# Performance work log

Measured on AMD Instinct MI355X. Metric: run time of the kernel, lower is better.

## Reference

```python
import jax, jax.numpy as jnp
import numpy as np

D_MODEL, D_STATE, D_CONV, EXPAND, DT_RANK = 2048, 16, 4, 2, 128
D_INNER = EXPAND * D_MODEL
BATCH, SEQLEN = 4, 2048


def setup_inputs() -> dict:
    key = jax.random.key(0)
    ks = jax.random.split(key, 10)
    s = lambda fan_in: 1.0 / np.sqrt(fan_in)
    hidden_states = jax.random.normal(ks[0], (BATCH, SEQLEN, D_MODEL), jnp.float32)
    W_in = jax.random.normal(ks[1], (2 * D_INNER, D_MODEL), jnp.float32) * s(D_MODEL)
    conv_w = jax.random.normal(ks[2], (D_INNER, D_CONV), jnp.float32) * s(D_CONV)
    conv_b = jax.random.normal(ks[3], (D_INNER,), jnp.float32) * 0.02
    W_x = jax.random.normal(ks[4], (DT_RANK + 2 * D_STATE, D_INNER), jnp.float32) * s(D_INNER)
    W_dt = jax.random.normal(ks[5], (D_INNER, DT_RANK), jnp.float32) * s(DT_RANK)
    # dt bias init so softplus(dt+bias) lands in a realistic small-dt range
    dt = jnp.exp(jax.random.uniform(ks[6], (D_INNER,)) * (np.log(0.1) - np.log(1e-3)) + np.log(1e-3))
    dt_bias = dt + jnp.log(-jnp.expm1(-dt))  # inverse softplus
    # A = -[1..d_state] per channel (standard S4D-real init)
    A_log = jnp.log(jnp.tile(jnp.arange(1, D_STATE + 1, dtype=jnp.float32), (D_INNER, 1)))
    D = jnp.ones((D_INNER,), jnp.float32)
    W_out = jax.random.normal(ks[7], (D_MODEL, D_INNER), jnp.float32) * s(D_INNER)
    return dict(hidden_states=hidden_states, W_in=W_in, conv_w=conv_w, conv_b=conv_b,
                W_x=W_x, W_dt=W_dt, dt_bias=dt_bias, A_log=A_log, D=D, W_out=W_out)


def _mamba_forward(hidden_states, W_in, conv_w, conv_b, W_x, W_dt, dt_bias, A_log, D, W_out):
    B_, L, _ = hidden_states.shape
    d_inner, d_state = A_log.shape
    dt_rank = W_dt.shape[1]

    # in_proj: (B,L,2*d_inner)
    xz = jnp.einsum('bld,ed->ble', hidden_states, W_in)
    x, z = jnp.split(xz, 2, axis=-1)              # each (B,L,d_inner)

    # depthwise causal conv1d over time
    x_bdl = jnp.transpose(x, (0, 2, 1))           # (B,d_inner,L)
    x_conv = jax.lax.conv_general_dilated(
        x_bdl, conv_w[:, None, :], window_strides=(1,),
        padding=[(conv_w.shape[-1] - 1, 0)],
        feature_group_count=d_inner,
        dimension_numbers=('NCH', 'OIH', 'NCH'))
    x_conv = x_conv + conv_b[None, :, None]
    xact = jax.nn.silu(jnp.transpose(x_conv, (0, 2, 1)))   # (B,L,d_inner)

    # x_proj -> dt, B, C
    x_dbl = jnp.einsum('bld,ed->ble', xact, W_x)
    dt_lr, Bm, Cm = jnp.split(x_dbl, [dt_rank, dt_rank + d_state], axis=-1)
    dt = jnp.einsum('blr,dr->bld', dt_lr, W_dt)            # (B,L,d_inner)
    delta = jax.nn.softplus(dt + dt_bias)                   # (B,L,d_inner)

    A = -jnp.exp(A_log)                                     # (d_inner,d_state)

    # selective scan over time (time-major xs)
    def step(h, inp):
        u_t, dlt_t, b_t, c_t = inp                          # (B,d),(B,d),(B,n),(B,n)
        dA = jnp.exp(dlt_t[..., None] * A)                  # (B,d,n)
        h = h * dA + (dlt_t * u_t)[..., None] * b_t[:, None, :]
        y_t = jnp.einsum('bdn,bn->bd', h, c_t)
        return h, y_t

    xs = (jnp.transpose(xact, (1, 0, 2)),
          jnp.transpose(delta, (1, 0, 2)),
          jnp.transpose(Bm, (1, 0, 2)),
          jnp.transpose(Cm, (1, 0, 2)))
    h0 = jnp.zeros((B_, d_inner, d_state), xact.dtype)
    _, ys = jax.lax.scan(step, h0, xs)                      # ys: (L,B,d_inner)
    y = jnp.transpose(ys, (1, 0, 2)) + D * xact             # skip via D
    y = y * jax.nn.silu(z)                                  # gating

    return jnp.einsum('bld,od->blo', y, W_out)              # out_proj


def reference(hidden_states, W_in, conv_w, conv_b, W_x, W_dt, dt_bias, A_log, D, W_out):
    return _mamba_forward(hidden_states, W_in, conv_w, conv_b, W_x, W_dt,
                          dt_bias, A_log, D, W_out)
```

## Files before the change

### kernel.cpp

```cpp
#include <hip/hip_runtime.h>
#include <hip/hip_bf16.h>
#include <math.h>

#define D_MODEL 2048
#define D_STATE 16
#define D_CONV  4
#define DT_RANK 128
#define D_INNER 4096
#define BATCH   4
#define SEQLEN  2048
#define BL      (BATCH * SEQLEN)

#define NCHUNK 8
#define CHUNK  (SEQLEN / NCHUNK)
#define SCH    32
#define NTILE  (CHUNK / SCH)

typedef __hip_bfloat16 bf16;
typedef __attribute__((ext_vector_type(8))) short  short8;
typedef __attribute__((ext_vector_type(4))) float  f32x4;

__device__ __forceinline__ float bf2f(bf16 v) { return __bfloat162float(v); }
__device__ __forceinline__ bf16  f2bf(float v) { return __float2bfloat16(v); }
__device__ __forceinline__ float us2f(unsigned short v) {
    return __uint_as_float((unsigned)v << 16);
}
__device__ __forceinline__ void st1(float* p, float v) { *p = v; }
__device__ __forceinline__ void st1(bf16* p, float v)  { *p = f2bf(v); }
__device__ __forceinline__ float fast_rcp(float x) { return __builtin_amdgcn_rcpf(x); }

__device__ __forceinline__ void async_cp16(const void* g, void* l) {
    __builtin_amdgcn_global_load_lds(
        (const __attribute__((address_space(1))) void*)g,
        (__attribute__((address_space(3))) void*)l, 16, 0, 0);
}

__device__ __forceinline__ float quad_sum(float p) {
    int q;
    q = __builtin_amdgcn_update_dpp(0, __float_as_int(p), 0xB1, 0xF, 0xF, false);
    p += __int_as_float(q);
    q = __builtin_amdgcn_update_dpp(0, __float_as_int(p), 0x4E, 0xF, 0xF, false);
    p += __int_as_float(q);
    return p;
}

template <int EPI, typename TC>
__global__ __launch_bounds__(256) void gemm_mfma_nt(
    const bf16* __restrict__ A, const bf16* __restrict__ B,
    TC* __restrict__ C, int M, int N, int K, int lda, int ldb, int ldc,
    const float* __restrict__ bias, bf16* __restrict__ aux,
    float* __restrict__ aux2)
{
    __shared__ bf16 As[128][64];
    __shared__ bf16 Bs[128][64];

    const int tid  = threadIdx.x;
    const int lane = tid & 63;
    const int wave = tid >> 6;
    const int wm   = (wave >> 1) * 64;
    const int wn   = (wave & 1) * 64;

    const int m0 = blockIdx.x * 128;
    const int n0 = blockIdx.y * 128;

    f32x4 acc[4][4] = {};

    const int srow = lane >> 3;
    const int scol = (lane & 7) * 8;

    for (int k0 = 0; k0 < K; k0 += 64) {
        __syncthreads();
#pragma unroll
        for (int i = 0; i < 4; ++i) {
            int seg = wave * 4 + i;
            int row = seg * 8 + srow;
            async_cp16(A + (size_t)(m0 + row) * lda + k0 + scol, &As[seg * 8][0]);
            async_cp16(B + (size_t)(n0 + row) * ldb + k0 + scol, &Bs[seg * 8][0]);
        }
        __syncthreads();

#pragma unroll
        for (int kk = 0; kk < 64; kk += 32) {
            short8 a[4], b[4];
            const int fr = lane & 15;
            const int fk = kk + (lane >> 4) * 8;
#pragma unroll
            for (int i = 0; i < 4; ++i) {
                a[i] = *(const short8*)&As[wm + i * 16 + fr][fk];
                b[i] = *(const short8*)&Bs[wn + i * 16 + fr][fk];
            }
#pragma unroll
            for (int i = 0; i < 4; ++i)
#pragma unroll
                for (int j = 0; j < 4; ++j)
                    acc[i][j] = __builtin_amdgcn_mfma_f32_16x16x32_bf16(
                        a[i], b[j], acc[i][j], 0, 0, 0);
        }
    }

#pragma unroll
    for (int i = 0; i < 4; ++i) {
        int row = m0 + wm + i * 16 + (lane >> 4) * 4;
#pragma unroll
        for (int j = 0; j < 4; ++j) {
            int col = n0 + wn + j * 16 + (lane & 15);
#pragma unroll
            for (int r = 0; r < 4; ++r) {
                float v = acc[i][j][r];
                if (EPI == 0) {
                    st1(C + (size_t)(row + r) * ldc + col, v);
                } else if (EPI == 1) {
                    if (col < DT_RANK)
                        aux[(size_t)(row + r) * DT_RANK + col] = f2bf(v);
                    else if (col < DT_RANK + 2 * D_STATE)
                        aux2[(size_t)(row + r) * (2 * D_STATE) + (col - DT_RANK)] = v;
                } else {
                    float x  = v + bias[col];
                    float sp = fmaxf(x, 0.f) + __logf(1.f + __expf(-fabsf(x)));
                    ((bf16*)C)[(size_t)(row + r) * ldc + col] = f2bf(sp);
                }
            }
        }
    }
}

__global__ void cvt_f32_bf16(const float* __restrict__ src,
                             bf16* __restrict__ dst, int n)
{
    int i = (blockIdx.x * blockDim.x + threadIdx.x) * 4;
    if (i >= n) return;
    float4 v = *(const float4*)(src + i);
    bf16 o[4] = { f2bf(v.x), f2bf(v.y), f2bf(v.z), f2bf(v.w) };
    *(ushort4*)(dst + i) = *(ushort4*)o;
}

__global__ void cvt_pad_wx(const float* __restrict__ src, bf16* __restrict__ dst)
{
    int i = (blockIdx.x * blockDim.x + threadIdx.x) * 4;
    if (i >= 256 * D_INNER) return;
    int row = i / D_INNER;
    bf16 o[4] = {};
    if (row < DT_RANK + 2 * D_STATE) {
        float4 v = *(const float4*)(src + i);
        o[0] = f2bf(v.x); o[1] = f2bf(v.y); o[2] = f2bf(v.z); o[3] = f2bf(v.w);
    }
    *(ushort4*)(dst + i) = *(ushort4*)o;
}

__global__ void conv_silu(const bf16* __restrict__ X,
                          const float* __restrict__ conv_w,
                          const float* __restrict__ conv_b,
                          bf16* __restrict__ xact)
{
    unsigned idx = blockIdx.x * blockDim.x + threadIdx.x;
    if (idx >= (unsigned)BL * (D_INNER / 8)) return;
    int c8 = (idx & (D_INNER / 8 - 1)) * 8;
    unsigned bl = idx >> 9;
    int l = bl & (SEQLEN - 1);
    int b = bl >> 11;

    float acc[8];
    float4 wv[8];
#pragma unroll
    for (int j = 0; j < 8; ++j) {
        acc[j] = conv_b[c8 + j];
        wv[j]  = *(const float4*)(conv_w + (c8 + j) * 4);
    }
#pragma unroll
    for (int t = 0; t < D_CONV; ++t) {
        int ll = l - (D_CONV - 1) + t;
        if (ll >= 0) {
            short8 xv = *(const short8*)(X + ((size_t)b * SEQLEN + ll) * D_INNER + c8);
#pragma unroll
            for (int j = 0; j < 8; ++j)
                acc[j] = fmaf(us2f((unsigned short)xv[j]), (&wv[j].x)[t], acc[j]);
        }
    }
    bf16 o[8];
#pragma unroll
    for (int j = 0; j < 8; ++j)
        o[j] = f2bf(acc[j] * fast_rcp(1.f + __expf(-acc[j])));
    *(short8*)(xact + (size_t)bl * D_INNER + c8) = *(short8*)o;
}

__global__ __launch_bounds__(256, 6) void scan_part1(
    const bf16* __restrict__ U,
    const bf16* __restrict__ DLT,
    const float* __restrict__ BC,
    const float* __restrict__ A_log,
    float4* __restrict__ Hscr,
    float*  __restrict__ Sscr)
{
    __shared__ unsigned short Us[2][SCH][64];
    __shared__ unsigned short Ds[2][SCH][64];

    const int b    = blockIdx.y;
    const int c    = blockIdx.z;
    const int d0   = blockIdx.x * 64;
    const int lane = threadIdx.x & 63;
    const int wave = threadIdx.x >> 6;
    const int sub  = lane & 3;
    const int grp  = lane >> 2;
    const int ci   = wave * 16 + grp;
    const int d    = d0 + ci;

    const float4 al = *(const float4*)&A_log[(size_t)d * D_STATE + 4 * sub];
    const float A0 = -__expf(al.x), A1 = -__expf(al.y),
                A2 = -__expf(al.z), A3 = -__expf(al.w);

    const size_t base = (size_t)b * SEQLEN + (size_t)c * CHUNK;

    const int sr = lane >> 3;
    const int sc = (lane & 7) * 8;

    auto stage = [&](int bb, int l0) {
        if (wave == 0) {
#pragma unroll
            for (int i = 0; i < 4; ++i) {
                int row = i * 8 + sr;
                async_cp16(U + (base + l0 + row) * (size_t)D_INNER + d0 + sc,
                           &Us[bb][i * 8][0]);
            }
        } else if (wave == 1) {
#pragma unroll
            for (int i = 0; i < 4; ++i) {
                int row = i * 8 + sr;
                async_cp16(DLT + (base + l0 + row) * (size_t)D_INNER + d0 + sc,
                           &Ds[bb][i * 8][0]);
            }
        }
    };

    float h0 = 0.f, h1 = 0.f, h2 = 0.f, h3 = 0.f, sdl = 0.f;

    stage(0, 0);
    __syncthreads();

    for (int t = 0; t < NTILE; ++t) {
        const int cur = t & 1, nxt = cur ^ 1;
        if (t + 1 < NTILE) stage(nxt, (t + 1) * SCH);

#pragma unroll 8
        for (int l = 0; l < SCH; ++l) {
            float u  = us2f(Us[cur][l][ci]);
            float dl = us2f(Ds[cur][l][ci]);
            float4 Bv = *(const float4*)(BC + (base + t * SCH + l) * (2 * D_STATE)
                                         + 4 * sub);
            float du = dl * u;
            h0 = fmaf(h0, __expf(dl * A0), du * Bv.x);
            h1 = fmaf(h1, __expf(dl * A1), du * Bv.y);
            h2 = fmaf(h2, __expf(dl * A2), du * Bv.z);
            h3 = fmaf(h3, __expf(dl * A3), du * Bv.w);
            sdl += dl;
        }
        __syncthreads();
    }

    const size_t idx = (size_t)(c * BATCH + b) * D_INNER + d;
    Hscr[idx * 4 + sub] = make_float4(h0, h1, h2, h3);
    if (sub == 0) Sscr[idx] = sdl;
}

__global__ void scan_combine(float4* __restrict__ Hscr,
                             const float* __restrict__ Sscr,
                             const float* __restrict__ A_log)
{
    int tid = blockIdx.x * blockDim.x + threadIdx.x;
    if (tid >= BATCH * D_INNER * 4) return;
    const int sub = tid & 3;
    const int d   = (tid >> 2) & (D_INNER - 1);
    const int b   = tid >> 14;

    const float4 al = *(const float4*)&A_log[(size_t)d * D_STATE + 4 * sub];
    const float A0 = -__expf(al.x), A1 = -__expf(al.y),
                A2 = -__expf(al.z), A3 = -__expf(al.w);

    float H0 = 0.f, H1 = 0.f, H2 = 0.f, H3 = 0.f;
#pragma unroll
    for (int c = 0; c < NCHUNK - 1; ++c) {
        const size_t idx = (size_t)(c * BATCH + b) * D_INNER + d;
        float4 hl = Hscr[idx * 4 + sub];
        float  s  = Sscr[idx];
        H0 = fmaf(H0, __expf(A0 * s), hl.x);
        H1 = fmaf(H1, __expf(A1 * s), hl.y);
        H2 = fmaf(H2, __expf(A2 * s), hl.z);
        H3 = fmaf(H3, __expf(A3 * s), hl.w);
        Hscr[idx * 4 + sub] = make_float4(H0, H1, H2, H3);
    }
}

__global__ __launch_bounds__(256, 6) void scan_main(
    const bf16* __restrict__ U,
    const bf16* __restrict__ DLT,
    const bf16* __restrict__ Z,
    const float* __restrict__ BC,
    const float* __restrict__ A_log,
    const float* __restrict__ Dp,
    const float4* __restrict__ Hscr,
    bf16* __restrict__ Y)
{
    __shared__ unsigned short Us[2][SCH][64];
    __shared__ unsigned short Ds[2][SCH][64];

    const int b    = blockIdx.y;
    const int c    = blockIdx.z;
    const int d0   = blockIdx.x * 64;
    const int lane = threadIdx.x & 63;
    const int wave = threadIdx.x >> 6;
    const int sub  = lane & 3;
    const int grp  = lane >> 2;
    const int ci   = wave * 16 + grp;
    const int d    = d0 + ci;

    const float4 al = *(const float4*)&A_log[(size_t)d * D_STATE + 4 * sub];
    const float A0 = -__expf(al.x), A1 = -__expf(al.y),
                A2 = -__expf(al.z), A3 = -__expf(al.w);
    const float Dv = Dp[d];

    const size_t base = (size_t)b * SEQLEN + (size_t)c * CHUNK;

    const int sr = lane >> 3;
    const int sc = (lane & 7) * 8;

    auto stage = [&](int bb, int l0) {
        if (wave == 0) {
#pragma unroll
            for (int i = 0; i < 4; ++i) {
                int row = i * 8 + sr;
                async_cp16(U + (base + l0 + row) * (size_t)D_INNER + d0 + sc,
                           &Us[bb][i * 8][0]);
            }
        } else if (wave == 1) {
#pragma unroll
            for (int i = 0; i < 4; ++i) {
                int row = i * 8 + sr;
                async_cp16(DLT + (base + l0 + row) * (size_t)D_INNER + d0 + sc,
                           &Ds[bb][i * 8][0]);
            }
        }
    };

    float h0 = 0.f, h1 = 0.f, h2 = 0.f, h3 = 0.f;
    if (c > 0) {
        float4 hi = Hscr[((size_t)((c - 1) * BATCH + b) * D_INNER + d) * 4 + sub];
        h0 = hi.x; h1 = hi.y; h2 = hi.z; h3 = hi.w;
    }

    stage(0, 0);
    __syncthreads();

    for (int t = 0; t < NTILE; ++t) {
        const int cur = t & 1, nxt = cur ^ 1;
        if (t + 1 < NTILE) stage(nxt, (t + 1) * SCH);

#pragma unroll 8
        for (int l = 0; l < SCH; ++l) {
            float u  = us2f(Us[cur][l][ci]);
            float dl = us2f(Ds[cur][l][ci]);
            const size_t tok = base + t * SCH + l;
            const float* bcp = BC + tok * (2 * D_STATE);
            float4 Bv = *(const float4*)(bcp + 4 * sub);
            float4 Cv = *(const float4*)(bcp + D_STATE + 4 * sub);
            float du = dl * u;
            h0 = fmaf(h0, __expf(dl * A0), du * Bv.x);
            h1 = fmaf(h1, __expf(dl * A1), du * Bv.y);
            h2 = fmaf(h2, __expf(dl * A2), du * Bv.z);
            h3 = fmaf(h3, __expf(dl * A3), du * Bv.w);
            float p = fmaf(h3, Cv.w, fmaf(h2, Cv.z, fmaf(h1, Cv.y, h0 * Cv.x)));
            p = quad_sum(p);
            float z = us2f(*(const unsigned short*)(Z + tok * (size_t)D_INNER + d));
            if (sub == 0) {
                float g = z * fast_rcp(1.f + __expf(-z));
                Y[tok * (size_t)D_INNER + d] = f2bf((p + Dv * u) * g);
            }
        }
        __syncthreads();
    }
}

extern "C" void kernel_launch(void* const* d_in, const int* in_sizes, int n_in,
                              void* d_out, int out_size, void* d_ws, size_t ws_size,
                              hipStream_t stream)
{
    const float* hs      = (const float*)d_in[0];
    const float* W_in    = (const float*)d_in[1];
    const float* conv_w  = (const float*)d_in[2];
    const float* conv_b  = (const float*)d_in[3];
    const float* W_x     = (const float*)d_in[4];
    const float* W_dt    = (const float*)d_in[5];
    const float* dt_bias = (const float*)d_in[6];
    const float* A_log   = (const float*)d_in[7];
    const float* Dp      = (const float*)d_in[8];
    const float* W_out   = (const float*)d_in[9];
    float* out = (float*)d_out;

    const size_t nBig = (size_t)BL * D_INNER;
    const size_t need = 2 * nBig * sizeof(bf16)
                      + (size_t)BL * 160 * sizeof(float);
    if (ws_size < need) {
        hipMemsetAsync(d_out, 0, (size_t)out_size * sizeof(float), stream);
        return;
    }

    bf16*  buf1  = (bf16*)d_ws;
    bf16*  buf2  = buf1 + nBig;
    float* BCbuf = (float*)(buf2 + nBig);
    bf16*  dtlr  = (bf16*)(BCbuf + (size_t)BL * 2 * D_STATE);
    bf16*  wxp   = dtlr + (size_t)BL * DT_RANK;
    bf16*  wdtb  = wxp;

    float4* Hscr = (float4*)dtlr;
    float*  Sscr = (float*)(Hscr + (size_t)(NCHUNK - 1) * BATCH * D_INNER * 4);

    const int nHS = BL * D_MODEL;
    const int nWI = 2 * D_INNER * D_MODEL;
    const int nWH = D_INNER * D_MODEL;
    bf16* hsb  = (bf16*)d_out;
    bf16* wb   = hsb + nHS;
    bf16* xact = (bf16*)d_out;

    cvt_f32_bf16<<<nHS / 1024, 256, 0, stream>>>(hs, hsb, nHS);
    cvt_f32_bf16<<<nWI / 1024, 256, 0, stream>>>(W_in, wb, nWI);
    gemm_mfma_nt<0, bf16><<<dim3(BL / 128, D_INNER / 128), 256, 0, stream>>>(
        hsb, wb + (size_t)nWH, buf2, BL, D_INNER, D_MODEL,
        D_MODEL, D_MODEL, D_INNER, nullptr, nullptr, nullptr);
    gemm_mfma_nt<0, bf16><<<dim3(BL / 128, D_INNER / 128), 256, 0, stream>>>(
        hsb, wb, buf1, BL, D_INNER, D_MODEL,
        D_MODEL, D_MODEL, D_INNER, nullptr, nullptr, nullptr);

    conv_silu<<<(BL * (D_INNER / 8)) / 256, 256, 0, stream>>>(
        buf1, conv_w, conv_b, xact);

    cvt_pad_wx<<<(256 * D_INNER) / 1024, 256, 0, stream>>>(W_x, wxp);
    gemm_mfma_nt<1, float><<<dim3(BL / 128, 2), 256, 0, stream>>>(
        xact, wxp, (float*)nullptr, BL, 256, D_INNER,
        D_INNER, D_INNER, 0, nullptr, dtlr, BCbuf);

    cvt_f32_bf16<<<(D_INNER * DT_RANK) / 1024, 256, 0, stream>>>(W_dt, wdtb,
                                                                 D_INNER * DT_RANK);
    gemm_mfma_nt<2, bf16><<<dim3(BL / 128, D_INNER / 128), 256, 0, stream>>>(
        dtlr, wdtb, buf1, BL, D_INNER, DT_RANK,
        DT_RANK, DT_RANK, D_INNER, dt_bias, nullptr, nullptr);

    scan_part1<<<dim3(D_INNER / 64, BATCH, NCHUNK - 1), 256, 0, stream>>>(
        xact, buf1, BCbuf, A_log, Hscr, Sscr);
    scan_combine<<<(BATCH * D_INNER * 4) / 256, 256, 0, stream>>>(
        Hscr, Sscr, A_log);
    scan_main<<<dim3(D_INNER / 64, BATCH, NCHUNK), 256, 0, stream>>>(
        xact, buf1, buf2, BCbuf, A_log, Dp, Hscr, buf2);

    cvt_f32_bf16<<<nWH / 1024, 256, 0, stream>>>(W_out, buf1, nWH);
    gemm_mfma_nt<0, float><<<dim3(BL / 128, D_MODEL / 128), 256, 0, stream>>>(
        buf2, buf1, out, BL, D_MODEL, D_INNER,
        D_INNER, D_INNER, D_MODEL, nullptr, nullptr, nullptr);
}
```

Before: 1.407 ms.

## Remap scan threads to 2 lanes per channel and drop LDS staging

Result: slower. 1.479 ms (+5.1%).

```diff
diff --git a/kernel.cpp b/kernel.cpp
--- a/kernel.cpp
+++ b/kernel.cpp
@@ -13,8 +13,6 @@
 
 #define NCHUNK 8
 #define CHUNK  (SEQLEN / NCHUNK)
-#define SCH    32
-#define NTILE  (CHUNK / SCH)
 
 typedef __hip_bfloat16 bf16;
 typedef __attribute__((ext_vector_type(8))) short  short8;
@@ -25,9 +23,17 @@
 __device__ __forceinline__ float us2f(unsigned short v) {
     return __uint_as_float((unsigned)v << 16);
 }
+__device__ __forceinline__ unsigned short f2us(float v) {
+    bf16 t = __float2bfloat16(v);
+    unsigned short u;
+    __builtin_memcpy(&u, &t, 2);
+    return u;
+}
 __device__ __forceinline__ void st1(float* p, float v) { *p = v; }
 __device__ __forceinline__ void st1(bf16* p, float v)  { *p = f2bf(v); }
 __device__ __forceinline__ float fast_rcp(float x) { return __builtin_amdgcn_rcpf(x); }
+__device__ __forceinline__ float fast_exp2(float x) { return __builtin_amdgcn_exp2f(x); }
+#define LOG2E 1.442695040888963f
 
 __device__ __forceinline__ void async_cp16(const void* g, void* l) {
     __builtin_amdgcn_global_load_lds(
@@ -35,13 +41,9 @@
         (__attribute__((address_space(3))) void*)l, 16, 0, 0);
 }
 
-__device__ __forceinline__ float quad_sum(float p) {
-    int q;
-    q = __builtin_amdgcn_update_dpp(0, __float_as_int(p), 0xB1, 0xF, 0xF, false);
-    p += __int_as_float(q);
-    q = __builtin_amdgcn_update_dpp(0, __float_as_int(p), 0x4E, 0xF, 0xF, false);
-    p += __int_as_float(q);
-    return p;
+__device__ __forceinline__ float pair_sum(float p) {
+    int q = __builtin_amdgcn_update_dpp(0, __float_as_int(p), 0xB1, 0xF, 0xF, false);
+    return p + __int_as_float(q);
 }
 
 template <int EPI, typename TC>
@@ -183,7 +185,7 @@
     *(short8*)(xact + (size_t)bl * D_INNER + c8) = *(short8*)o;
 }
 
-__global__ __launch_bounds__(256, 6) void scan_part1(
+__global__ __launch_bounds__(256, 4) void scan_part1(
     const bf16* __restrict__ U,
     const bf16* __restrict__ DLT,
     const float* __restrict__ BC,
@@ -191,74 +193,56 @@
     float4* __restrict__ Hscr,
     float*  __restrict__ Sscr)
 {
-    __shared__ unsigned short Us[2][SCH][64];
-    __shared__ unsigned short Ds[2][SCH][64];
-
     const int b    = blockIdx.y;
     const int c    = blockIdx.z;
-    const int d0   = blockIdx.x * 64;
+    const int d0   = blockIdx.x * 128;
     const int lane = threadIdx.x & 63;
     const int wave = threadIdx.x >> 6;
-    const int sub  = lane & 3;
-    const int grp  = lane >> 2;
-    const int ci   = wave * 16 + grp;
+    const int s2   = lane & 1;
+    const int ci   = wave * 32 + (lane >> 1);
     const int d    = d0 + ci;
 
-    const float4 al = *(const float4*)&A_log[(size_t)d * D_STATE + 4 * sub];
-    const float A0 = -__expf(al.x), A1 = -__expf(al.y),
-                A2 = -__expf(al.z), A3 = -__expf(al.w);
+    float A2[8], h[8];
+    {
+        float4 a0 = *(const float4*)&A_log[(size_t)d * D_STATE + 8 * s2];
+        float4 a1 = *(const float4*)&A_log[(size_t)d * D_STATE + 8 * s2 + 4];
+        A2[0] = -__expf(a0.x) * LOG2E; A2[1] = -__expf(a0.y) * LOG2E;
+        A2[2] = -__expf(a0.z) * LOG2E; A2[3] = -__expf(a0.w) * LOG2E;
+        A2[4] = -__expf(a1.x) * LOG2E; A2[5] = -__expf(a1.y) * LOG2E;
+        A2[6] = -__expf(a1.z) * LOG2E; A2[7] = -__expf(a1.w) * LOG2E;
+#pragma unroll
+        for (int j = 0; j < 8; ++j) h[j] = 0.f;
+    }
 
     const size_t base = (size_t)b * SEQLEN + (size_t)c * CHUNK;
-
-    const int sr = lane >> 3;
-    const int sc = (lane & 7) * 8;
-
-    auto stage = [&](int bb, int l0) {
-        if (wave == 0) {
-#pragma unroll
-            for (int i = 0; i < 4; ++i) {
-                int row = i * 8 + sr;
-                async_cp16(U + (base + l0 + row) * (size_t)D_INNER + d0 + sc,
-                           &Us[bb][i * 8][0]);
-            }
-        } else if (wave == 1) {
-#pragma unroll
-            for (int i = 0; i < 4; ++i) {
-                int row = i * 8 + sr;
-                async_cp16(DLT + (base + l0 + row) * (size_t)D_INNER + d0 + sc,
-                           &Ds[bb][i * 8][0]);
-            }
-        }
-    };
-
-    float h0 = 0.f, h1 = 0.f, h2 = 0.f, h3 = 0.f, sdl = 0.f;
-
-    stage(0, 0);
-    __syncthreads();
-
-    for (int t = 0; t < NTILE; ++t) {
-        const int cur = t & 1, nxt = cur ^ 1;
-        if (t + 1 < NTILE) stage(nxt, (t + 1) * SCH);
-
-#pragma unroll 8
-        for (int l = 0; l < SCH; ++l) {
-            float u  = us2f(Us[cur][l][ci]);
-            float dl = us2f(Ds[cur][l][ci]);
-            float4 Bv = *(const float4*)(BC + (base + t * SCH + l) * (2 * D_STATE)
-                                         + 4 * sub);
-            float du = dl * u;
-            h0 = fmaf(h0, __expf(dl * A0), du * Bv.x);
-            h1 = fmaf(h1, __expf(dl * A1), du * Bv.y);
-            h2 = fmaf(h2, __expf(dl * A2), du * Bv.z);
-            h3 = fmaf(h3, __expf(dl * A3), du * Bv.w);
-            sdl += dl;
-        }
-        __syncthreads();
+    const unsigned short* up  = (const unsigned short*)U   + base * D_INNER + d;
+    const unsigned short* dp  = (const unsigned short*)DLT + base * D_INNER + d;
+    const float*          bcp = BC + base * (2 * D_STATE) + 8 * s2;
+
+    float sdl = 0.f;
+
+#pragma unroll 4
+    for (int l = 0; l < CHUNK; ++l) {
+        float u  = us2f(up[(size_t)l * D_INNER]);
+        float dl = us2f(dp[(size_t)l * D_INNER]);
+        float4 B0 = *(const float4*)(bcp + (size_t)l * 32);
+        float4 B1 = *(const float4*)(bcp + (size_t)l * 32 + 4);
+        float du = dl * u;
+        h[0] = fmaf(h[0], fast_exp2(dl * A2[0]), du * B0.x);
+        h[1] = fmaf(h[1], fast_exp2(dl * A2[1]), du * B0.y);
+        h[2] = fmaf(h[2], fast_exp2(dl * A2[2]), du * B0.z);
+        h[3] = fmaf(h[3], fast_exp2(dl * A2[3]), du * B0.w);
+        h[4] = fmaf(h[4], fast_exp2(dl * A2[4]), du * B1.x);
+        h[5] = fmaf(h[5], fast_exp2(dl * A2[5]), du * B1.y);
+        h[6] = fmaf(h[6], fast_exp2(dl * A2[6]), du * B1.z);
+        h[7] = fmaf(h[7], fast_exp2(dl * A2[7]), du * B1.w);
+        sdl += dl;
     }
 
     const size_t idx = (size_t)(c * BATCH + b) * D_INNER + d;
-    Hscr[idx * 4 + sub] = make_float4(h0, h1, h2, h3);
-    if (sub == 0) Sscr[idx] = sdl;
+    Hscr[idx * 4 + 2 * s2]     = make_float4(h[0], h[1], h[2], h[3]);
+    Hscr[idx * 4 + 2 * s2 + 1] = make_float4(h[4], h[5], h[6], h[7]);
+    if (s2 == 0) Sscr[idx] = sdl;
 }
 
 __global__ void scan_combine(float4* __restrict__ Hscr,
@@ -289,7 +273,7 @@
     }
 }
 
-__global__ __launch_bounds__(256, 6) void scan_main(
+__global__ __launch_bounds__(256, 4) void scan_main(
     const bf16* __restrict__ U,
     const bf16* __restrict__ DLT,
     const bf16* __restrict__ Z,
@@ -299,82 +283,72 @@
     const float4* __restrict__ Hscr,
     bf16* __restrict__ Y)
 {
-    __shared__ unsigned short Us[2][SCH][64];
-    __shared__ unsigned short Ds[2][SCH][64];
-
     const int b    = blockIdx.y;
     const int c    = blockIdx.z;
-    const int d0   = blockIdx.x * 64;
+    const int d0   = blockIdx.x * 128;
     const int lane = threadIdx.x & 63;
     const int wave = threadIdx.x >> 6;
-    const int sub  = lane & 3;
-    const int grp  = lane >> 2;
-    const int ci   = wave * 16 + grp;
+    const int s2   = lane & 1;
+    const int ci   = wave * 32 + (lane >> 1);
     const int d    = d0 + ci;
 
-    const float4 al = *(const float4*)&A_log[(size_t)d * D_STATE + 4 * sub];
-    const float A0 = -__expf(al.x), A1 = -__expf(al.y),
-                A2 = -__expf(al.z), A3 = -__expf(al.w);
+    float A2[8], h[8];
+    {
+        float4 a0 = *(const float4*)&A_log[(size_t)d * D_STATE + 8 * s2];
+        float4 a1 = *(const float4*)&A_log[(size_t)d * D_STATE + 8 * s2 + 4];
+        A2[0] = -__expf(a0.x) * LOG2E; A2[1] = -__expf(a0.y) * LOG2E;
+        A2[2] = -__expf(a0.z) * LOG2E; A2[3] = -__expf(a0.w) * LOG2E;
+        A2[4] = -__expf(a1.x) * LOG2E; A2[5] = -__expf(a1.y) * LOG2E;
+        A2[6] = -__expf(a1.z) * LOG2E; A2[7] = -__expf(a1.w) * LOG2E;
+    }
     const float Dv = Dp[d];
 
+    if (c > 0) {
+        const size_t hidx = ((size_t)((c - 1) * BATCH + b) * D_INNER + d) * 4 + 2 * s2;
+        float4 h0q = Hscr[hidx];
+        float4 h1q = Hscr[hidx + 1];
+        h[0] = h0q.x; h[1] = h0q.y; h[2] = h0q.z; h[3] = h0q.w;
+        h[4] = h1q.x; h[5] = h1q.y; h[6] = h1q.z; h[7] = h1q.w;
+    } else {
+#pragma unroll
+        for (int j = 0; j < 8; ++j) h[j] = 0.f;
+    }
+
     const size_t base = (size_t)b * SEQLEN + (size_t)c * CHUNK;
-
-    const int sr = lane >> 3;
-    const int sc = (lane & 7) * 8;
-
-    auto stage = [&](int bb, int l0) {
-        if (wave == 0) {
-#pragma unroll
-            for (int i = 0; i < 4; ++i) {
-                int row = i * 8 + sr;
-                async_cp16(U + (base + l0 + row) * (size_t)D_INNER + d0 + sc,
-                           &Us[bb][i * 8][0]);
-            }
-        } else if (wave == 1) {
-#pragma unroll
-            for (int i = 0; i < 4; ++i) {
-                int row = i * 8 + sr;
-                async_cp16(DLT + (base + l0 + row) * (size_t)D_INNER + d0 + sc,
-                           &Ds[bb][i * 8][0]);
-            }
+    const unsigned short* up  = (const unsigned short*)U   + base * D_INNER + d;
+    const unsigned short* dp  = (const unsigned short*)DLT + base * D_INNER + d;
+    const unsigned short* zp  = (const unsigned short*)Z   + base * D_INNER + d;
+    unsigned short*       yp  = (unsigned short*)Y         + base * D_INNER + d;
+    const float*          bcp = BC + base * (2 * D_STATE) + 8 * s2;
+
+#pragma unroll 4
+    for (int l = 0; l < CHUNK; ++l) {
+        float u  = us2f(up[(size_t)l * D_INNER]);
+        float dl = us2f(dp[(size_t)l * D_INNER]);
+        float z  = us2f(zp[(size_t)l * D_INNER]);
+        float4 B0 = *(const float4*)(bcp + (size_t)l * 32);
+        float4 B1 = *(const float4*)(bcp + (size_t)l * 32 + 4);
+        float4 C0 = *(const float4*)(bcp + (size_t)l * 32 + D_STATE);
+        float4 C1 = *(const float4*)(bcp + (size_t)l * 32 + D_STATE + 4);
+        float du = dl * u;
+        h[0] = fmaf(h[0], fast_exp2(dl * A2[0]), du * B0.x);
+        h[1] = fmaf(h[1], fast_exp2(dl * A2[1]), du * B0.y);
+        h[2] = fmaf(h[2], fast_exp2(dl * A2[2]), du * B0.z);
+        h[3] = fmaf(h[3], fast_exp2(dl * A2[3]), du * B0.w);
+        h[4] = fmaf(h[4], fast_exp2(dl * A2[4]), du * B1.x);
+        h[5] = fmaf(h[5], fast_exp2(dl * A2[5]), du * B1.y);
+        h[6] = fmaf(h[6], fast_exp2(dl * A2[6]), du * B1.z);
+        h[7] = fmaf(h[7], fast_exp2(dl * A2[7]), du * B1.w);
+        float p01 = fmaf(h[1], C0.y, h[0] * C0.x);
+        float p23 = fmaf(h[3], C0.w, h[2] * C0.z);
+        float p45 = fmaf(h[5], C1.y, h[4] * C1.x);
+        float p67 = fmaf(h[7], C1.w, h[6] * C1.z);
+        float p = (p01 + p23) + (p45 + p67);
+        p = pair_sum(p);
+        if (s2 == 0) {
+            float g = z * fast_rcp(1.f + fast_exp2(-LOG2E * z));
+            yp[(size_t)l * D_INNER] = f2us((p + Dv * u) * g);
         }
-    };
-
-    float h0 = 0.f, h1 = 0.f, h2 = 0.f, h3 = 0.f;
-    if (c > 0) {
-        float4 hi = Hscr[((size_t)((c - 1) * BATCH + b) * D_INNER + d) * 4 + sub];
-        h0 = hi.x; h1 = hi.y; h2 = hi.z; h3 = hi.w;
-    }
-
-    stage(0, 0);
-    __syncthreads();
-
-    for (int t = 0; t < NTILE; ++t) {
-        const int cur = t & 1, nxt = cur ^ 1;
-        if (t + 1 < NTILE) stage(nxt, (t + 1) * SCH);
-
-#pragma unroll 8
-        for (int l = 0; l < SCH; ++l) {
-            float u  = us2f(Us[cur][l][ci]);
-            float dl = us2f(Ds[cur][l][ci]);
-            const size_t tok = base + t * SCH + l;
-            const float* bcp = BC + tok * (2 * D_STATE);
-            float4 Bv = *(const float4*)(bcp + 4 * sub);
-            float4 Cv = *(const float4*)(bcp + D_STATE + 4 * sub);
-            float du = dl * u;
-            h0 = fmaf(h0, __expf(dl * A0), du * Bv.x);
-            h1 = fmaf(h1, __expf(dl * A1), du * Bv.y);
-            h2 = fmaf(h2, __expf(dl * A2), du * Bv.z);
-            h3 = fmaf(h3, __expf(dl * A3), du * Bv.w);
-            float p = fmaf(h3, Cv.w, fmaf(h2, Cv.z, fmaf(h1, Cv.y, h0 * Cv.x)));
-            p = quad_sum(p);
-            float z = us2f(*(const unsigned short*)(Z + tok * (size_t)D_INNER + d));
-            if (sub == 0) {
-                float g = z * fast_rcp(1.f + __expf(-z));
-                Y[tok * (size_t)D_INNER + d] = f2bf((p + Dv * u) * g);
-            }
-        }
-        __syncthreads();
     }
 }
 
@@ -398,7 +372,7 @@
     const size_t need = 2 * nBig * sizeof(bf16)
                       + (size_t)BL * 160 * sizeof(float);
     if (ws_size < need) {
-        hipMemsetAsync(d_out, 0, (size_t)out_size * sizeof(float), stream);
+        (void)hipMemsetAsync(d_out, 0, (size_t)out_size * sizeof(float), stream);
         return;
     }
 
@@ -442,11 +416,11 @@
         dtlr, wdtb, buf1, BL, D_INNER, DT_RANK,
         DT_RANK, DT_RANK, D_INNER, dt_bias, nullptr, nullptr);
 
-    scan_part1<<<dim3(D_INNER / 64, BATCH, NCHUNK - 1), 256, 0, stream>>>(
+    scan_part1<<<dim3(D_INNER / 128, BATCH, NCHUNK - 1), 256, 0, stream>>>(
         xact, buf1, BCbuf, A_log, Hscr, Sscr);
     scan_combine<<<(BATCH * D_INNER * 4) / 256, 256, 0, stream>>>(
         Hscr, Sscr, A_log);
-    scan_main<<<dim3(D_INNER / 64, BATCH, NCHUNK), 256, 0, stream>>>(
+    scan_main<<<dim3(D_INNER / 128, BATCH, NCHUNK), 256, 0, stream>>>(
         xact, buf1, buf2, BCbuf, A_log, Dp, Hscr, buf2);
 
     cvt_f32_bf16<<<nWH / 1024, 256, 0, stream>>>(W_out, buf1, nWH);
```
